# Performance work log

Measured on AMD Instinct MI355X. Metric: run time of the kernel, lower is better.

Reference implementation:

```python
import jax, jax.numpy as jnp
import numpy as np
import math

V, D, L, FF, H, DH, W, DM, T, B = 32000, 1024, 4, 4096, 16, 64, 256, 64, 1024, 1


def rms_norm(x, w):
    return x * jax.lax.rsqrt(jnp.mean(x * x, axis=-1, keepdims=True) + 1e-6) * w


def setup_inputs() -> dict:
    key = jax.random.key(0)
    ks = jax.random.split(key, 16)
    s = 0.02
    return {
        "x": jax.random.randint(ks[0], (B, T), 0, V),
        "embed": jax.random.normal(ks[1], (V, D), jnp.float32) * s,
        "ln_in_w": jnp.ones((D,), jnp.float32),
        "ln1_w": jnp.ones((L, D), jnp.float32),
        "lnd_w": jnp.ones((L, D), jnp.float32),
        "qkv_w": jax.random.normal(ks[2], (L, 3 * H * DH, D), jnp.float32) * s,
        "swa_out_w": jax.random.normal(ks[3], (L, D, H * DH), jnp.float32) * s,
        "k_w": jax.random.normal(ks[4], (L, H * DM, D), jnp.float32) * s,
        "v_w": jax.random.normal(ks[5], (L, H * DM, D), jnp.float32) * s,
        "q_w": jax.random.normal(ks[6], (L, H * DM, D), jnp.float32) * s,
        "beta_w": jax.random.normal(ks[7], (L, H, D), jnp.float32) * s,
        "mem_out_w": jax.random.normal(ks[8], (L, D, H * DM), jnp.float32) * s,
        "gate_w": jax.random.normal(ks[9], (L, D, D), jnp.float32) * s,
        "comb_w": jax.random.normal(ks[10], (L, D, D), jnp.float32) * s,
        "ln2_w": jnp.ones((L, D), jnp.float32),
        "wg": jax.random.normal(ks[11], (L, FF, D), jnp.float32) * s,
        "wu": jax.random.normal(ks[12], (L, FF, D), jnp.float32) * s,
        "wo": jax.random.normal(ks[13], (L, D, FF), jnp.float32) * s,
        "ln_out_w": jnp.ones((D,), jnp.float32),
    }


def _swa(h1, qkv_w, out_w):
    # h1: [B,T,D]
    qkv = jnp.einsum('btd,ed->bte', h1, qkv_w)  # [B,T,3*H*DH]
    q, k, v = jnp.split(qkv, 3, axis=-1)
    q = q.reshape(h1.shape[0], T, H, DH).transpose(0, 2, 1, 3)
    k = k.reshape(h1.shape[0], T, H, DH).transpose(0, 2, 1, 3)
    v = v.reshape(h1.shape[0], T, H, DH).transpose(0, 2, 1, 3)
    scores = jnp.einsum('bhqd,bhkd->bhqk', q, k) * (DH ** -0.5)
    pos = jnp.arange(T)
    dist = pos[:, None] - pos[None, :]
    allowed = (dist >= 0) & (dist < W)  # causal sliding window
    scores = jnp.where(allowed[None, None], scores, -jnp.inf)
    attn = jax.nn.softmax(scores, axis=-1)
    out = jnp.einsum('bhqk,bhkd->bhqd', attn, v)
    out = out.transpose(0, 2, 1, 3).reshape(h1.shape[0], T, H * DH)
    return jnp.einsum('bte,de->btd', out, out_w)


def _delta(h2, k_w, v_w, q_w, beta_w, mem_out_w):
    Bv = h2.shape[0]
    proj = lambda w: jnp.einsum('btd,ed->bte', h2, w).reshape(Bv, T, H, DM).transpose(0, 2, 1, 3)
    keys, values, queries = proj(k_w), proj(v_w), proj(q_w)
    beta = jax.nn.sigmoid(jnp.einsum('btd,hd->bht', h2, beta_w))  # [B,H,T]
    keys = keys / jnp.maximum(jnp.linalg.norm(keys, axis=-1, keepdims=True), 1e-12)
    queries = queries / jnp.maximum(jnp.linalg.norm(queries, axis=-1, keepdims=True), 1e-12)
    log_retain = jnp.log(1.0 - beta + 1e-8)
    cum_log = jnp.cumsum(log_retain, axis=-1)  # [B,H,T]
    log_decay = cum_log[..., :, None] - cum_log[..., None, :]  # [B,H,T,T]
    causal = jnp.triu(jnp.ones((T, T), dtype=bool))  # matches torch.triu mask in source
    decay = jnp.exp(jnp.minimum(log_decay, 0.0)) * causal
    kq = jnp.einsum('bhid,bhjd->bhij', queries, keys) / math.sqrt(DM)
    weights = kq * decay
    out = jnp.einsum('bhij,bhjd->bhid', weights, values)
    out = out + beta[..., None] * values
    out = out.transpose(0, 2, 1, 3).reshape(Bv, T, H * DM)
    return jnp.einsum('bte,de->btd', out, mem_out_w)


def reference(x, embed, ln_in_w, ln1_w, lnd_w, qkv_w, swa_out_w, k_w, v_w, q_w,
              beta_w, mem_out_w, gate_w, comb_w, ln2_w, wg, wu, wo, ln_out_w):
    h = rms_norm(embed[x], ln_in_w)  # [B,T,D]
    for l in range(L):
        h1 = rms_norm(h, ln1_w[l])
        h2 = rms_norm(h, lnd_w[l])
        local = _swa(h1, qkv_w[l], swa_out_w[l])
        global_ctx = _delta(h2, k_w[l], v_w[l], q_w[l], beta_w[l], mem_out_w[l])
        gate = jax.nn.sigmoid(jnp.einsum('btd,ed->bte', h1, gate_w[l]))
        mixed = jnp.einsum('btd,ed->bte', gate * local + (1.0 - gate) * global_ctx, comb_w[l])
        h = h + mixed
        hn = rms_norm(h, ln2_w[l])
        ffn = jnp.einsum('btf,df->btd', jax.nn.silu(jnp.einsum('btd,fd->btf', hn, wg[l])) * jnp.einsum('btd,fd->btf', hn, wu[l]), wo[l])
        h = h + ffn
    logits = jnp.einsum('btd,vd->btv', rms_norm(h, ln_out_w), embed)  # tied head
    return logits
```

## Files before the change

### kernel.cpp

```cpp
#include <hip/hip_runtime.h>

typedef unsigned short u16;
typedef unsigned int   u32;
typedef __attribute__((ext_vector_type(8))) __bf16 bfv8;
typedef __attribute__((ext_vector_type(4))) float  f32x4;

__device__ __forceinline__ u16 f2bf(float f){
  u32 u = __builtin_bit_cast(u32, f);
  return (u16)((u + 0x7FFFu + ((u >> 16) & 1u)) >> 16);
}
__device__ __forceinline__ float bf2f(u16 b){
  return __builtin_bit_cast(float, ((u32)b) << 16);
}
__device__ __forceinline__ u32 pk2(float a, float b){
  return (u32)f2bf(a) | ((u32)f2bf(b) << 16);
}
__device__ __forceinline__ float wsum(float v){
  #pragma unroll
  for (int m = 32; m > 0; m >>= 1) v += __shfl_xor(v, m, 64);
  return v;
}
__device__ __forceinline__ void gload16(const void* g, void* l){
  __builtin_amdgcn_global_load_lds((const __attribute__((address_space(1))) void*)g,
                                   (__attribute__((address_space(3))) void*)l, 16, 0, 0);
}

struct CBatch { const float* s[12]; long long p4[13]; u16* dst; };
__global__ __launch_bounds__(256) void flm_conv(CBatch cb)
{
  const int seg = blockIdx.y;
  const long long base = cb.p4[seg];
  const long long n4 = cb.p4[seg + 1] - base;
  const float* __restrict__ src = cb.s[seg];
  uint2* __restrict__ dst = (uint2*)cb.dst + base;
  for (long long i = (long long)blockIdx.x * 256 + threadIdx.x; i < n4;
       i += (long long)gridDim.x * 256){
    float4 v = ((const float4*)src)[i];
    uint2 p; p.x = pk2(v.x, v.y); p.y = pk2(v.z, v.w);
    dst[i] = p;
  }
}

struct GDesc {
  const u16* A; const float* Bw; float* Cf; u16* Cb;
  int lda, ldb, ldc, kbeg, kend, blk0, epi, pad;
};
struct GBatch { GDesc d[6]; int ng, total; };

template<bool BW>
__global__ __launch_bounds__(512) void flm_mgemm(GBatch gb)
{
  constexpr int LDK = BW ? 64 : 72;
  __shared__ u16 sA[128][LDK];
  __shared__ u16 sB[128][LDK];
  const int tid = threadIdx.x, lane = tid & 63, w = tid >> 6;

  const int T = gb.total, bid = blockIdx.x;
  const int q8 = T >> 3, r8 = T & 7, xc = bid & 7, of = bid >> 3;
  const int lin = (xc < r8 ? xc * (q8 + 1) : r8 * (q8 + 1) + (xc - r8) * q8) + of;
  int di = 0;
  #pragma unroll
  for (int i = 1; i < 6; i++) if (i < gb.ng && lin >= gb.d[i].blk0) di = i;
  const GDesc g = gb.d[di];
  const int local = lin - g.blk0;
  const int row0 = (local & 7) * 128;
  const int col0 = (local >> 3) * 128;
  const int wr = (w >> 2) * 64, wc = (w & 3) * 32;

  f32x4 acc[4][2];
  #pragma unroll
  for (int m = 0; m < 4; m++)
    #pragma unroll
    for (int n = 0; n < 2; n++)
      acc[m][n] = (f32x4){0.f, 0.f, 0.f, 0.f};

  const int csw = ((lane & 7) ^ (lane >> 3)) * 8;
  const u16* B16 = (const u16*)g.Bw;

  for (int k0 = g.kbeg; k0 < g.kend; k0 += 64){
    if constexpr (BW){
      const u16* a0 = g.A + (size_t)(row0 + w*16 + (lane>>3)) * g.lda + k0 + csw;
      const u16* b0 = B16 + (size_t)(col0 + w*16 + (lane>>3)) * g.ldb + k0 + csw;
      gload16(a0,                     &sA[w*16    ][0]);
      gload16(a0 + (size_t)8*g.lda,   &sA[w*16 + 8][0]);
      gload16(b0,                     &sB[w*16    ][0]);
      gload16(b0 + (size_t)8*g.ldb,   &sB[w*16 + 8][0]);
    } else {
      #pragma unroll
      for (int i = 0; i < 2; i++){
        int idx = tid + i * 512;
        int r = idx >> 3, c = (idx & 7) * 8;
        *(uint4*)&sA[r][c] = *(const uint4*)(g.A + (size_t)(row0 + r) * g.lda + k0 + c);
      }
      #pragma unroll
      for (int i = 0; i < 4; i++){
        int idx = tid + i * 512;
        int r = idx >> 4, c = (idx & 15) * 4;
        float4 v = *(const float4*)(g.Bw + (size_t)(col0 + r) * g.ldb + k0 + c);
        uint2 p; p.x = pk2(v.x, v.y); p.y = pk2(v.z, v.w);
        *(uint2*)&sB[r][c] = p;
      }
    }
    __syncthreads();
    #pragma unroll
    for (int kk = 0; kk < 2; kk++){
      bfv8 af[4], bfr[2];
      #pragma unroll
      for (int m = 0; m < 4; m++){
        int row = wr + m*16 + (lane & 15);
        if constexpr (BW){
          int slot = (kk*4 + (lane >> 4)) ^ (row & 7);
          af[m] = *(const bfv8*)((const char*)sA + row*128 + slot*16);
        } else {
          af[m] = *(const bfv8*)&sA[row][kk*32 + (lane >> 4) * 8];
        }
      }
      #pragma unroll
      for (int n = 0; n < 2; n++){
        int row = wc + n*16 + (lane & 15);
        if constexpr (BW){
          int slot = (kk*4 + (lane >> 4)) ^ (row & 7);
          bfr[n] = *(const bfv8*)((const char*)sB + row*128 + slot*16);
        } else {
          bfr[n] = *(const bfv8*)&sB[row][kk*32 + (lane >> 4) * 8];
        }
      }
      #pragma unroll
      for (int m = 0; m < 4; m++)
        #pragma unroll
        for (int n = 0; n < 2; n++)
          acc[m][n] = __builtin_amdgcn_mfma_f32_16x16x32_bf16(af[m], bfr[n], acc[m][n], 0, 0, 0);
    }
    __syncthreads();
  }

  #pragma unroll
  for (int m = 0; m < 4; m++){
    int rbase = row0 + wr + m*16 + (lane >> 4) * 4;
    #pragma unroll
    for (int n = 0; n < 2; n++){
      int col = col0 + wc + n*16 + (lane & 15);
      #pragma unroll
      for (int j = 0; j < 4; j++){
        float v = acc[m][n][j];
        size_t o = (size_t)(rbase + j) * g.ldc + col;
        switch (g.epi){
          case 0: g.Cf[o] = v; break;
          case 1: g.Cb[o] = f2bf(v); break;
          default: atomicAdd(&g.Cf[o], v); break;
        }
      }
    }
  }
}

__global__ __launch_bounds__(256) void flm_mix(
    const float* __restrict__ gr, const float* __restrict__ lo,
    const float* __restrict__ gl, u16* __restrict__ o)
{
  int i = blockIdx.x * 256 + threadIdx.x;
  float4 gv = ((const float4*)gr)[i];
  float4 lv = ((const float4*)lo)[i];
  float4 bv = ((const float4*)gl)[i];
  float sx = 1.f/(1.f+expf(-gv.x)), sy = 1.f/(1.f+expf(-gv.y));
  float sz = 1.f/(1.f+expf(-gv.z)), sw = 1.f/(1.f+expf(-gv.w));
  uint2 p;
  p.x = pk2(sx*lv.x + (1.f-sx)*bv.x, sy*lv.y + (1.f-sy)*bv.y);
  p.y = pk2(sz*lv.z + (1.f-sz)*bv.z, sw*lv.w + (1.f-sw)*bv.w);
  ((uint2*)o)[i] = p;
}

__global__ __launch_bounds__(256) void flm_silu(
    const u16* __restrict__ gg, const u16* __restrict__ uu, u16* __restrict__ o)
{
  int i = blockIdx.x * 256 + threadIdx.x;
  uint2 gv = ((const uint2*)gg)[i];
  uint2 uv = ((const uint2*)uu)[i];
  float g0 = bf2f((u16)gv.x), g1 = bf2f((u16)(gv.x >> 16));
  float g2 = bf2f((u16)gv.y), g3 = bf2f((u16)(gv.y >> 16));
  float u0 = bf2f((u16)uv.x), u1 = bf2f((u16)(uv.x >> 16));
  float u2 = bf2f((u16)uv.y), u3 = bf2f((u16)(uv.y >> 16));
  float a = g0 / (1.f + expf(-g0)) * u0;
  float b = g1 / (1.f + expf(-g1)) * u1;
  float c = g2 / (1.f + expf(-g2)) * u2;
  float d = g3 / (1.f + expf(-g3)) * u3;
  uint2 p; p.x = pk2(a, b); p.y = pk2(c, d);
  ((uint2*)o)[i] = p;
}

__global__ __launch_bounds__(256) void flm_embed(
    const int* __restrict__ x, const float* __restrict__ embed,
    const float* __restrict__ w, float* __restrict__ h)
{
  int t = blockIdx.x, tid = threadIdx.x;
  int tok = x[t];
  float4 v = ((const float4*)(embed + (size_t)tok * 1024))[tid];
  float ss = v.x*v.x + v.y*v.y + v.z*v.z + v.w*v.w;
  ss = wsum(ss);
  __shared__ float red[4];
  if ((tid & 63) == 0) red[tid >> 6] = ss;
  __syncthreads();
  float inv = rsqrtf((red[0]+red[1]+red[2]+red[3]) * (1.f/1024.f) + 1e-6f);
  float4 wv = ((const float4*)w)[tid];
  float4 o; o.x = v.x*inv*wv.x; o.y = v.y*inv*wv.y; o.z = v.z*inv*wv.z; o.w = v.w*inv*wv.w;
  ((float4*)(h + (size_t)t * 1024))[tid] = o;
}

__global__ __launch_bounds__(256) void flm_rms(
    const float* __restrict__ h, const float* __restrict__ w1, const float* __restrict__ w2,
    u16* __restrict__ o1, u16* __restrict__ o2)
{
  int t = blockIdx.x, tid = threadIdx.x;
  float4 v = ((const float4*)(h + (size_t)t * 1024))[tid];
  float ss = v.x*v.x + v.y*v.y + v.z*v.z + v.w*v.w;
  ss = wsum(ss);
  __shared__ float red[4];
  if ((tid & 63) == 0) red[tid >> 6] = ss;
  __syncthreads();
  float inv = rsqrtf((red[0]+red[1]+red[2]+red[3]) * (1.f/1024.f) + 1e-6f);
  {
    float4 wv = ((const float4*)w1)[tid];
    uint2 p; p.x = pk2(v.x*inv*wv.x, v.y*inv*wv.y); p.y = pk2(v.z*inv*wv.z, v.w*inv*wv.w);
    ((uint2*)(o1 + (size_t)t * 1024))[tid] = p;
  }
  if (o2 != nullptr){
    float4 wv = ((const float4*)w2)[tid];
    uint2 p; p.x = pk2(v.x*inv*wv.x, v.y*inv*wv.y); p.y = pk2(v.z*inv*wv.z, v.w*inv*wv.w);
    ((uint2*)(o2 + (size_t)t * 1024))[tid] = p;
  }
}

__global__ __launch_bounds__(64) void flm_betanorm(
    const u16* __restrict__ h2, const float* __restrict__ bw, float* __restrict__ beta,
    u16* __restrict__ keys, u16* __restrict__ queries)
{
  int t = blockIdx.x, lane = threadIdx.x;
  float hv[16];
  #pragma unroll
  for (int i = 0; i < 16; i++) hv[i] = bf2f(h2[(size_t)t*1024 + i*64 + lane]);
  for (int h = 0; h < 16; h++){
    float p = 0.f;
    #pragma unroll
    for (int i = 0; i < 16; i++) p += hv[i] * bw[h*1024 + i*64 + lane];
    p = wsum(p);
    if (lane == 0) beta[t*16 + h] = 1.f / (1.f + expf(-p));
  }
  #pragma unroll
  for (int h = 0; h < 16; h++){
    size_t idx = (size_t)t * 1024 + h * 64 + lane;
    float v = bf2f(keys[idx]);
    float nrm = fmaxf(sqrtf(wsum(v * v)), 1e-12f);
    keys[idx] = f2bf(v / nrm);
    float q = bf2f(queries[idx]);
    float qn = fmaxf(sqrtf(wsum(q * q)), 1e-12f);
    queries[idx] = f2bf(q / qn);
  }
}

__global__ __launch_bounds__(256) void flm_attn(
    const u16* __restrict__ qkv,
    const u16* __restrict__ keys, const u16* __restrict__ values, const u16* __restrict__ queries,
    const float* __restrict__ beta, u16* __restrict__ aout, u16* __restrict__ dout)
{
  __shared__ u16 sK[64][72];
  __shared__ u16 sVt[64][72];
  __shared__ u16 sP[4][16][72];
  const int tid = threadIdx.x, lane = tid & 63, w = tid >> 6;
  const int qt = blockIdx.x, h = blockIdx.y;
  const int base = h * 64;
  const int ri = w*16 + (lane>>4)*4;

  if (blockIdx.z == 0){
    bfv8 aq[2];
    {
      int qrow = qt*64 + w*16 + (lane & 15);
      #pragma unroll
      for (int kk = 0; kk < 2; kk++)
        aq[kk] = *(const bfv8*)(qkv + (size_t)qrow*3072 + base + kk*32 + (lane>>4)*8);
    }
    f32x4 acc_o[4];
    float m_r[4], l_r[4];
    #pragma unroll
    for (int n = 0; n < 4; n++) acc_o[n] = (f32x4){0.f,0.f,0.f,0.f};
    #pragma unroll
    for (int r = 0; r < 4; r++){ m_r[r] = -1e30f; l_r[r] = 0.f; }
    const int jt0 = (qt >= 4) ? qt - 4 : 0;

    for (int jt = qt; jt >= jt0; jt--){
      #pragma unroll
      for (int i = 0; i < 2; i++){
        int idx = tid + i*256;
        int r = idx >> 3, c = (idx & 7) * 8;
        uint4 kv = *(const uint4*)(qkv + (size_t)(jt*64+r)*3072 + 1024 + base + c);
        *(uint4*)&sK[r][c] = kv;
        uint4 vv = *(const uint4*)(qkv + (size_t)(jt*64+r)*3072 + 2048 + base + c);
        u16 tmp[8]; *(uint4*)tmp = vv;
        #pragma unroll
        for (int e = 0; e < 8; e++) sVt[c+e][r] = tmp[e];
      }
      __syncthreads();

      f32x4 sv[4];
      #pragma unroll
      for (int n = 0; n < 4; n++) sv[n] = (f32x4){0.f,0.f,0.f,0.f};
      #pragma unroll
      for (int kk = 0; kk < 2; kk++){
        #pragma unroll
        for (int n = 0; n < 4; n++){
          bfv8 bk = *(const bfv8*)&sK[n*16 + (lane & 15)][(lane>>4)*8 + kk*32];
          sv[n] = __builtin_amdgcn_mfma_f32_16x16x32_bf16(aq[kk], bk, sv[n], 0, 0, 0);
        }
      }
      #pragma unroll
      for (int n = 0; n < 4; n++){
        int cj = n*16 + (lane & 15);
        #pragma unroll
        for (int r = 0; r < 4; r++){
          float s = sv[n][r] * 0.125f;
          if (jt == qt)      { if (cj > ri + r) s = -1e30f; }
          else if (jt == jt0 && qt - jt0 == 4) { if (cj <= ri + r) s = -1e30f; }
          sv[n][r] = s;
        }
      }
      float pv[4][4], scl[4];
      #pragma unroll
      for (int r = 0; r < 4; r++){
        float mx = -1e30f;
        #pragma unroll
        for (int n = 0; n < 4; n++) mx = fmaxf(mx, sv[n][r]);
        #pragma unroll
        for (int m = 1; m < 16; m <<= 1) mx = fmaxf(mx, __shfl_xor(mx, m, 64));
        float mn = fmaxf(m_r[r], mx);
        float sc = expf(m_r[r] - mn);
        m_r[r] = mn; scl[r] = sc;
        float rs = 0.f;
        #pragma unroll
        for (int n = 0; n < 4; n++){ float p = expf(sv[n][r] - mn); pv[n][r] = p; rs += p; }
        #pragma unroll
        for (int m = 1; m < 16; m <<= 1) rs += __shfl_xor(rs, m, 64);
        l_r[r] = l_r[r] * sc + rs;
      }
      #pragma unroll
      for (int n = 0; n < 4; n++){
        #pragma unroll
        for (int r = 0; r < 4; r++){
          acc_o[n][r] *= scl[r];
          sP[w][(lane>>4)*4 + r][n*16 + (lane & 15)] = f2bf(pv[n][r]);
        }
      }
      #pragma unroll
      for (int kk = 0; kk < 2; kk++){
        bfv8 ap = *(const bfv8*)&sP[w][lane & 15][(lane>>4)*8 + kk*32];
        #pragma unroll
        for (int n = 0; n < 4; n++){
          bfv8 bv = *(const bfv8*)&sVt[n*16 + (lane & 15)][(lane>>4)*8 + kk*32];
          acc_o[n] = __builtin_amdgcn_mfma_f32_16x16x32_bf16(ap, bv, acc_o[n], 0, 0, 0);
        }
      }
      __syncthreads();
    }

    #pragma unroll
    for (int n = 0; n < 4; n++){
      int col = base + n*16 + (lane & 15);
      #pragma unroll
      for (int r = 0; r < 4; r++){
        int row = qt*64 + ri + r;
        aout[(size_t)row*1024 + col] = f2bf(acc_o[n][r] / l_r[r]);
      }
    }
  } else {
    bfv8 aq[2];
    {
      int qrow = qt*64 + w*16 + (lane & 15);
      #pragma unroll
      for (int kk = 0; kk < 2; kk++)
        aq[kk] = *(const bfv8*)(queries + (size_t)qrow*1024 + base + kk*32 + (lane>>4)*8);
    }
    f32x4 acc_o[4];
    #pragma unroll
    for (int n = 0; n < 4; n++) acc_o[n] = (f32x4){0.f,0.f,0.f,0.f};

    for (int jt = qt; jt < 16; jt++){
      #pragma unroll
      for (int i = 0; i < 2; i++){
        int idx = tid + i*256;
        int r = idx >> 3, c = (idx & 7) * 8;
        uint4 kv = *(const uint4*)(keys + (size_t)(jt*64+r)*1024 + base + c);
        *(uint4*)&sK[r][c] = kv;
        uint4 vv = *(const uint4*)(values + (size_t)(jt*64+r)*1024 + base + c);
        u16 tmp[8]; *(uint4*)tmp = vv;
        #pragma unroll
        for (int e = 0; e < 8; e++) sVt[c+e][r] = tmp[e];
      }
      __syncthreads();

      f32x4 sv[4];
      #pragma unroll
      for (int n = 0; n < 4; n++) sv[n] = (f32x4){0.f,0.f,0.f,0.f};
      #pragma unroll
      for (int kk = 0; kk < 2; kk++){
        #pragma unroll
        for (int n = 0; n < 4; n++){
          bfv8 bk = *(const bfv8*)&sK[n*16 + (lane & 15)][(lane>>4)*8 + kk*32];
          sv[n] = __builtin_amdgcn_mfma_f32_16x16x32_bf16(aq[kk], bk, sv[n], 0, 0, 0);
        }
      }
      #pragma unroll
      for (int n = 0; n < 4; n++){
        int cj = n*16 + (lane & 15);
        #pragma unroll
        for (int r = 0; r < 4; r++){
          float p = sv[n][r] * 0.125f;
          if (jt == qt && cj < ri + r) p = 0.f;
          sP[w][(lane>>4)*4 + r][n*16 + (lane & 15)] = f2bf(p);
        }
      }
      #pragma unroll
      for (int kk = 0; kk < 2; kk++){
        bfv8 ap = *(const bfv8*)&sP[w][lane & 15][(lane>>4)*8 + kk*32];
        #pragma unroll
        for (int n = 0; n < 4; n++){
          bfv8 bv = *(const bfv8*)&sVt[n*16 + (lane & 15)][(lane>>4)*8 + kk*32];
          acc_o[n] = __builtin_amdgcn_mfma_f32_16x16x32_bf16(ap, bv, acc_o[n], 0, 0, 0);
        }
      }
      __syncthreads();
    }

    #pragma unroll
    for (int n = 0; n < 4; n++){
      int col = base + n*16 + (lane & 15);
      #pragma unroll
      for (int r = 0; r < 4; r++){
        int row = qt*64 + ri + r;
        float b = beta[row*16 + h];
        float v = bf2f(values[(size_t)row*1024 + col]);
        dout[(size_t)row*1024 + col] = f2bf(acc_o[n][r] + b * v);
      }
    }
  }
}

static GDesc mkd(const u16* A, int lda, const float* Bw, int ldb,
                 float* Cf, u16* Cb, int ldc,
                 int kbeg, int kend, int blk0, int epi){
  GDesc d; d.A=A; d.Bw=Bw; d.Cf=Cf; d.Cb=Cb;
  d.lda=lda; d.ldb=ldb; d.ldc=ldc; d.kbeg=kbeg; d.kend=kend; d.blk0=blk0; d.epi=epi; d.pad=0;
  return d;
}

extern "C" void kernel_launch(void* const* d_in, const int* in_sizes, int n_in,
                              void* d_out, int out_size, void* d_ws, size_t ws_size,
                              hipStream_t stream)
{
  (void)in_sizes; (void)n_in; (void)out_size;
  const int*   x        = (const int*)d_in[0];
  const float* embed    = (const float*)d_in[1];
  const float* ln_in_w  = (const float*)d_in[2];
  const float* ln1_w    = (const float*)d_in[3];
  const float* lnd_w    = (const float*)d_in[4];
  const float* qkv_w    = (const float*)d_in[5];
  const float* swa_out_w= (const float*)d_in[6];
  const float* k_w      = (const float*)d_in[7];
  const float* v_w      = (const float*)d_in[8];
  const float* q_w      = (const float*)d_in[9];
  const float* beta_w   = (const float*)d_in[10];
  const float* mem_out_w= (const float*)d_in[11];
  const float* gate_w   = (const float*)d_in[12];
  const float* comb_w   = (const float*)d_in[13];
  const float* ln2_w    = (const float*)d_in[14];
  const float* wg       = (const float*)d_in[15];
  const float* wu       = (const float*)d_in[16];
  const float* wo       = (const float*)d_in[17];
  const float* ln_out_w = (const float*)d_in[18];
  float* out = (float*)d_out;

  char* ws = (char*)d_ws;
  const size_t KB = 1024, MB = 1u << 20;
  float* h       = (float*)(ws + 0);
  u16*   h1      = (u16*)  (ws + 4*MB);
  u16*   h2      = (u16*)  (ws + 6*MB);
  u16*   qkvb    = (u16*)  (ws + 8*MB);
  u16*   keys    = (u16*)  (ws + 14*MB);
  u16*   values  = (u16*)  (ws + 16*MB);
  u16*   queries = (u16*)  (ws + 18*MB);
  float* beta    = (float*)(ws + 20*MB);
  u16*   attn    = (u16*)  (ws + 20*MB + 256*KB);
  u16*   delt    = (u16*)  (ws + 22*MB + 256*KB);
  float* localb  = (float*)(ws + 24*MB + 256*KB);
  float* globb   = (float*)(ws + 28*MB + 256*KB);
  u16*   mcomb   = (u16*)  (ws + 32*MB + 256*KB);
  u16*   hn      = (u16*)  (ws + 36*MB);
  float* gbuf    = (float*)(ws + 40*MB);
  u16*   g16     = (u16*)  (ws + 4*MB);
  u16*   u16b    = (u16*)  (ws + 12*MB);
  u16*   sbuf    = (u16*)  (ws + 36*MB);

  u16* wb = (u16*)(ws + 44*MB);
  size_t off = 0; auto nx = [&](size_t n){ size_t o = off; off += n; return o; };
  const size_t nEmb = 32768000ULL, nQkv = 12582912ULL, nSq = 4194304ULL, nFf = 16777216ULL;
  u16* wemb  = wb + nx(nEmb);
  u16* wqkv  = wb + nx(nQkv);
  u16* wswa  = wb + nx(nSq);
  u16* wk    = wb + nx(nSq);
  u16* wv    = wb + nx(nSq);
  u16* wq    = wb + nx(nSq);
  u16* wmem  = wb + nx(nSq);
  u16* wgate = wb + nx(nSq);
  u16* wcomb = wb + nx(nSq);
  u16* wwg   = wb + nx(nFf);
  u16* wwu   = wb + nx(nFf);
  u16* wwo   = wb + nx(nFf);
  const size_t NEED = 44*MB + off * 2;
  const bool bw = (ws_size >= NEED);

  auto MG = [&](int nblk, GBatch& gbv){
    if (bw) flm_mgemm<true><<<nblk, 512, 0, stream>>>(gbv);
    else    flm_mgemm<false><<<nblk, 512, 0, stream>>>(gbv);
  };

  if (bw){
    CBatch cb;
    const float* srcs[12] = {embed, qkv_w, swa_out_w, k_w, v_w, q_w,
                             mem_out_w, gate_w, comb_w, wg, wu, wo};
    const size_t ns[12] = {nEmb, nQkv, nSq, nSq, nSq, nSq, nSq, nSq, nSq, nFf, nFf, nFf};
    long long acc4 = 0;
    for (int i = 0; i < 12; i++){ cb.s[i] = srcs[i]; cb.p4[i] = acc4; acc4 += (long long)(ns[i] >> 2); }
    cb.p4[12] = acc4; cb.dst = wb;
    flm_conv<<<dim3(1024, 12), 256, 0, stream>>>(cb);
  }

  flm_embed<<<1024, 256, 0, stream>>>(x, embed, ln_in_w, h);

  for (int l = 0; l < 4; l++){
    const size_t lq = (size_t)l * 3145728, ls = (size_t)l * 1048576, lf = (size_t)l * 4194304;
    const float* Wqkv  = bw ? (const float*)(wqkv  + lq) : qkv_w     + lq;
    const float* Wk    = bw ? (const float*)(wk    + ls) : k_w       + ls;
    const float* Wv    = bw ? (const float*)(wv    + ls) : v_w       + ls;
    const float* Wq    = bw ? (const float*)(wq    + ls) : q_w       + ls;
    const float* Wswa  = bw ? (const float*)(wswa  + ls) : swa_out_w + ls;
    const float* Wmem  = bw ? (const float*)(wmem  + ls) : mem_out_w + ls;
    const float* Wgate = bw ? (const float*)(wgate + ls) : gate_w    + ls;
    const float* Wcomb = bw ? (const float*)(wcomb + ls) : comb_w    + ls;
    const float* Wwg   = bw ? (const float*)(wwg   + lf) : wg        + lf;
    const float* Wwu   = bw ? (const float*)(wwu   + lf) : wu        + lf;
    const float* Wwo   = bw ? (const float*)(wwo   + lf) : wo        + lf;

    flm_rms<<<1024, 256, 0, stream>>>(h, ln1_w + l*1024, lnd_w + l*1024, h1, h2);

    {
      GBatch gb;
      gb.d[0] = mkd(h1, 1024, Wqkv, 1024, nullptr, qkvb, 3072, 0, 1024, 0, 1);
      gb.d[1] = mkd(h2, 1024, Wk, 1024, nullptr, keys, 1024, 0, 1024, 192, 1);
      gb.d[2] = mkd(h2, 1024, Wv, 1024, nullptr, values, 1024, 0, 1024, 256, 1);
      gb.d[3] = mkd(h2, 1024, Wq, 1024, nullptr, queries, 1024, 0, 1024, 320, 1);
      gb.d[4] = mkd(h1, 1024, Wgate, 1024, gbuf, nullptr, 1024, 0, 1024, 384, 0);
      gb.d[5] = gb.d[4]; gb.d[5].blk0 = 0x7fffffff;
      gb.ng = 5; gb.total = 448;
      MG(448, gb);
    }
    flm_betanorm<<<1024, 64, 0, stream>>>(h2, beta_w + (size_t)l*16*1024, beta, keys, queries);
    flm_attn<<<dim3(16, 16, 2), 256, 0, stream>>>(qkvb, keys, values, queries, beta, attn, delt);

    {
      GBatch gb;
      gb.d[0] = mkd(attn, 1024, Wswa, 1024, localb, nullptr, 1024, 0, 1024, 0, 0);
      gb.d[1] = mkd(delt, 1024, Wmem, 1024, globb, nullptr, 1024, 0, 1024, 64, 0);
      gb.d[2] = gb.d[1]; gb.d[2].blk0 = 0x7fffffff;
      gb.d[3] = gb.d[2]; gb.d[4] = gb.d[2]; gb.d[5] = gb.d[2];
      gb.ng = 2; gb.total = 128;
      MG(128, gb);
    }
    flm_mix<<<1024, 256, 0, stream>>>(gbuf, localb, globb, mcomb);
    {
      GBatch gb;
      gb.d[0] = mkd(mcomb, 1024, Wcomb, 1024, h, nullptr, 1024, 0, 512, 0, 5);
      gb.d[1] = mkd(mcomb, 1024, Wcomb, 1024, h, nullptr, 1024, 512, 1024, 64, 5);
      gb.d[2] = gb.d[1]; gb.d[2].blk0 = 0x7fffffff;
      gb.d[3] = gb.d[2]; gb.d[4] = gb.d[2]; gb.d[5] = gb.d[2];
      gb.ng = 2; gb.total = 128;
      MG(128, gb);
    }
    flm_rms<<<1024, 256, 0, stream>>>(h, ln2_w + l*1024, nullptr, hn, nullptr);
    {
      GBatch gb;
      gb.d[0] = mkd(hn, 1024, Wwg, 1024, nullptr, g16, 4096, 0, 1024, 0, 1);
      gb.d[1] = mkd(hn, 1024, Wwu, 1024, nullptr, u16b, 4096, 0, 1024, 256, 1);
      gb.d[2] = gb.d[1]; gb.d[2].blk0 = 0x7fffffff;
      gb.d[3] = gb.d[2]; gb.d[4] = gb.d[2]; gb.d[5] = gb.d[2];
      gb.ng = 2; gb.total = 512;
      MG(512, gb);
    }
    flm_silu<<<4096, 256, 0, stream>>>(g16, u16b, sbuf);
    {
      GBatch gb;
      for (int s = 0; s < 4; s++)
        gb.d[s] = mkd(sbuf, 4096, Wwo, 4096, h, nullptr, 1024, s*1024, (s+1)*1024, s*64, 5);
      gb.d[4] = gb.d[3]; gb.d[4].blk0 = 0x7fffffff;
      gb.d[5] = gb.d[4];
      gb.ng = 4; gb.total = 256;
      MG(256, gb);
    }
  }

  flm_rms<<<1024, 256, 0, stream>>>(h, ln_out_w, nullptr, hn, nullptr);
  {
    GBatch gb;
    gb.d[0] = mkd(hn, 1024, bw ? (const float*)wemb : embed, 1024, out, nullptr, 32000,
                  0, 1024, 0, 0);
    gb.d[1] = gb.d[0]; gb.d[1].blk0 = 0x7fffffff;
    gb.d[2] = gb.d[1]; gb.d[3] = gb.d[1]; gb.d[4] = gb.d[1]; gb.d[5] = gb.d[1];
    gb.ng = 1; gb.total = 2000;
    MG(2000, gb);
  }
}
```

Before: 1.007 ms.

## Fuse gate-mix and SiLU into GEMM A-loads, split-K out-proj, balance delta attention

The elementwise gate/mix kernel and the SiLU*up kernel are folded into the A-operand staging of the following GEMMs (AF=1 and AF=2), which removes two launches and their intermediate round trips. The SWA/memory output projections become split-K with partial sums kept in separate buffers that the fused mix adds together. The delta-attention blocks now each process query tiles p and 15-p, so the triangular work per block is balanced, and the weight conversion kernel uses wider nontemporal loads and stores. The trade-off is that A-tile loads become synchronous register loads with expf computed inside the GEMM loop, and each K-step reads five fp32 arrays.

```diff
diff --git a/kernel.cpp b/kernel.cpp
--- a/kernel.cpp
+++ b/kernel.cpp
@@ -4,6 +4,7 @@
 typedef unsigned int   u32;
 typedef __attribute__((ext_vector_type(8))) __bf16 bfv8;
 typedef __attribute__((ext_vector_type(4))) float  f32x4;
+typedef __attribute__((ext_vector_type(4))) u32    u32x4;
 
 __device__ __forceinline__ u16 f2bf(float f){
   u32 u = __builtin_bit_cast(u32, f);
@@ -30,24 +31,28 @@
 {
   const int seg = blockIdx.y;
   const long long base = cb.p4[seg];
-  const long long n4 = cb.p4[seg + 1] - base;
-  const float* __restrict__ src = cb.s[seg];
-  uint2* __restrict__ dst = (uint2*)cb.dst + base;
-  for (long long i = (long long)blockIdx.x * 256 + threadIdx.x; i < n4;
+  const long long n8 = (cb.p4[seg + 1] - base) >> 1;
+  const f32x4* __restrict__ src = (const f32x4*)cb.s[seg];
+  u32x4* __restrict__ dst = (u32x4*)cb.dst + (base >> 1);
+  for (long long i = (long long)blockIdx.x * 256 + threadIdx.x; i < n8;
        i += (long long)gridDim.x * 256){
-    float4 v = ((const float4*)src)[i];
-    uint2 p; p.x = pk2(v.x, v.y); p.y = pk2(v.z, v.w);
-    dst[i] = p;
+    f32x4 v0 = __builtin_nontemporal_load(src + 2*i);
+    f32x4 v1 = __builtin_nontemporal_load(src + 2*i + 1);
+    u32x4 p;
+    p.x = pk2(v0.x, v0.y); p.y = pk2(v0.z, v0.w);
+    p.z = pk2(v1.x, v1.y); p.w = pk2(v1.z, v1.w);
+    __builtin_nontemporal_store(p, dst + i);
   }
 }
 
 struct GDesc {
   const u16* A; const float* Bw; float* Cf; u16* Cb;
+  const void* xa; const void* xb; const void* xc; const void* xd; const void* xe;
   int lda, ldb, ldc, kbeg, kend, blk0, epi, pad;
 };
 struct GBatch { GDesc d[6]; int ng, total; };
 
-template<bool BW>
+template<bool BW, int AF>
 __global__ __launch_bounds__(512) void flm_mgemm(GBatch gb)
 {
   constexpr int LDK = BW ? 64 : 72;
@@ -75,16 +80,54 @@
       acc[m][n] = (f32x4){0.f, 0.f, 0.f, 0.f};
 
   const int csw = ((lane & 7) ^ (lane >> 3)) * 8;
+  const int arow = w*16 + (lane >> 3);
   const u16* B16 = (const u16*)g.Bw;
 
   for (int k0 = g.kbeg; k0 < g.kend; k0 += 64){
     if constexpr (BW){
-      const u16* a0 = g.A + (size_t)(row0 + w*16 + (lane>>3)) * g.lda + k0 + csw;
-      const u16* b0 = B16 + (size_t)(col0 + w*16 + (lane>>3)) * g.ldb + k0 + csw;
-      gload16(a0,                     &sA[w*16    ][0]);
-      gload16(a0 + (size_t)8*g.lda,   &sA[w*16 + 8][0]);
-      gload16(b0,                     &sB[w*16    ][0]);
-      gload16(b0 + (size_t)8*g.ldb,   &sB[w*16 + 8][0]);
+      if constexpr (AF == 0){
+        const u16* a0 = g.A + (size_t)(row0 + arow) * g.lda + k0 + csw;
+        gload16(a0,                   &sA[w*16    ][0]);
+        gload16(a0 + (size_t)8*g.lda, &sA[w*16 + 8][0]);
+      } else if constexpr (AF == 1){
+        #pragma unroll
+        for (int half = 0; half < 2; half++){
+          int rr = arow + half*8;
+          size_t base = (size_t)(row0 + rr) * 1024 + k0 + csw;
+          const float* G  = (const float*)g.xa + base;
+          const float* L0 = (const float*)g.xb + base;
+          const float* L1 = (const float*)g.xc + base;
+          const float* H0 = (const float*)g.xd + base;
+          const float* H1 = (const float*)g.xe + base;
+          u16 t8[8];
+          #pragma unroll
+          for (int e = 0; e < 8; e++){
+            float s = 1.f / (1.f + expf(-G[e]));
+            t8[e] = f2bf(s * (L0[e] + L1[e]) + (1.f - s) * (H0[e] + H1[e]));
+          }
+          *(uint4*)&sA[rr][(lane & 7) * 8] = *(uint4*)t8;
+        }
+      } else {
+        #pragma unroll
+        for (int half = 0; half < 2; half++){
+          int rr = arow + half*8;
+          size_t base = (size_t)(row0 + rr) * g.lda + k0 + csw;
+          uint4 gv = *(const uint4*)((const u16*)g.xa + base);
+          uint4 uv = *(const uint4*)((const u16*)g.xb + base);
+          const u16* gp = (const u16*)&gv;
+          const u16* up = (const u16*)&uv;
+          u16 t8[8];
+          #pragma unroll
+          for (int e = 0; e < 8; e++){
+            float gg = bf2f(gp[e]), uu = bf2f(up[e]);
+            t8[e] = f2bf(gg / (1.f + expf(-gg)) * uu);
+          }
+          *(uint4*)&sA[rr][(lane & 7) * 8] = *(uint4*)t8;
+        }
+      }
+      const u16* b0 = B16 + (size_t)(col0 + arow) * g.ldb + k0 + csw;
+      gload16(b0,                   &sB[w*16    ][0]);
+      gload16(b0 + (size_t)8*g.ldb, &sB[w*16 + 8][0]);
     } else {
       #pragma unroll
       for (int i = 0; i < 2; i++){
@@ -266,11 +309,12 @@
   __shared__ u16 sVt[64][72];
   __shared__ u16 sP[4][16][72];
   const int tid = threadIdx.x, lane = tid & 63, w = tid >> 6;
-  const int qt = blockIdx.x, h = blockIdx.y;
+  const int bx = blockIdx.x, h = blockIdx.y;
   const int base = h * 64;
   const int ri = w*16 + (lane>>4)*4;
 
-  if (blockIdx.z == 0){
+  if (bx < 16){
+    const int qt = bx;
     bfv8 aq[2];
     {
       int qrow = qt*64 + w*16 + (lane & 15);
@@ -370,73 +414,78 @@
       }
     }
   } else {
-    bfv8 aq[2];
-    {
-      int qrow = qt*64 + w*16 + (lane & 15);
-      #pragma unroll
-      for (int kk = 0; kk < 2; kk++)
-        aq[kk] = *(const bfv8*)(queries + (size_t)qrow*1024 + base + kk*32 + (lane>>4)*8);
-    }
-    f32x4 acc_o[4];
-    #pragma unroll
-    for (int n = 0; n < 4; n++) acc_o[n] = (f32x4){0.f,0.f,0.f,0.f};
-
-    for (int jt = qt; jt < 16; jt++){
-      #pragma unroll
-      for (int i = 0; i < 2; i++){
-        int idx = tid + i*256;
-        int r = idx >> 3, c = (idx & 7) * 8;
-        uint4 kv = *(const uint4*)(keys + (size_t)(jt*64+r)*1024 + base + c);
-        *(uint4*)&sK[r][c] = kv;
-        uint4 vv = *(const uint4*)(values + (size_t)(jt*64+r)*1024 + base + c);
-        u16 tmp[8]; *(uint4*)tmp = vv;
-        #pragma unroll
-        for (int e = 0; e < 8; e++) sVt[c+e][r] = tmp[e];
-      }
-      __syncthreads();
-
-      f32x4 sv[4];
-      #pragma unroll
-      for (int n = 0; n < 4; n++) sv[n] = (f32x4){0.f,0.f,0.f,0.f};
-      #pragma unroll
-      for (int kk = 0; kk < 2; kk++){
+    const int p = bx - 16;
+    #pragma unroll 1
+    for (int sel = 0; sel < 2; sel++){
+      const int qt = sel ? (15 - p) : p;
+      bfv8 aq[2];
+      {
+        int qrow = qt*64 + w*16 + (lane & 15);
+        #pragma unroll
+        for (int kk = 0; kk < 2; kk++)
+          aq[kk] = *(const bfv8*)(queries + (size_t)qrow*1024 + base + kk*32 + (lane>>4)*8);
+      }
+      f32x4 acc_o[4];
+      #pragma unroll
+      for (int n = 0; n < 4; n++) acc_o[n] = (f32x4){0.f,0.f,0.f,0.f};
+
+      for (int jt = qt; jt < 16; jt++){
+        #pragma unroll
+        for (int i = 0; i < 2; i++){
+          int idx = tid + i*256;
+          int r = idx >> 3, c = (idx & 7) * 8;
+          uint4 kv = *(const uint4*)(keys + (size_t)(jt*64+r)*1024 + base + c);
+          *(uint4*)&sK[r][c] = kv;
+          uint4 vv = *(const uint4*)(values + (size_t)(jt*64+r)*1024 + base + c);
+          u16 tmp[8]; *(uint4*)tmp = vv;
+          #pragma unroll
+          for (int e = 0; e < 8; e++) sVt[c+e][r] = tmp[e];
+        }
+        __syncthreads();
+
+        f32x4 sv[4];
+        #pragma unroll
+        for (int n = 0; n < 4; n++) sv[n] = (f32x4){0.f,0.f,0.f,0.f};
+        #pragma unroll
+        for (int kk = 0; kk < 2; kk++){
+          #pragma unroll
+          for (int n = 0; n < 4; n++){
+            bfv8 bk = *(const bfv8*)&sK[n*16 + (lane & 15)][(lane>>4)*8 + kk*32];
+            sv[n] = __builtin_amdgcn_mfma_f32_16x16x32_bf16(aq[kk], bk, sv[n], 0, 0, 0);
+          }
+        }
         #pragma unroll
         for (int n = 0; n < 4; n++){
-          bfv8 bk = *(const bfv8*)&sK[n*16 + (lane & 15)][(lane>>4)*8 + kk*32];
-          sv[n] = __builtin_amdgcn_mfma_f32_16x16x32_bf16(aq[kk], bk, sv[n], 0, 0, 0);
-        }
-      }
+          int cj = n*16 + (lane & 15);
+          #pragma unroll
+          for (int r = 0; r < 4; r++){
+            float pp = sv[n][r] * 0.125f;
+            if (jt == qt && cj < ri + r) pp = 0.f;
+            sP[w][(lane>>4)*4 + r][n*16 + (lane & 15)] = f2bf(pp);
+          }
+        }
+        #pragma unroll
+        for (int kk = 0; kk < 2; kk++){
+          bfv8 ap = *(const bfv8*)&sP[w][lane & 15][(lane>>4)*8 + kk*32];
+          #pragma unroll
+          for (int n = 0; n < 4; n++){
+            bfv8 bv = *(const bfv8*)&sVt[n*16 + (lane & 15)][(lane>>4)*8 + kk*32];
+            acc_o[n] = __builtin_amdgcn_mfma_f32_16x16x32_bf16(ap, bv, acc_o[n], 0, 0, 0);
+          }
+        }
+        __syncthreads();
+      }
+
       #pragma unroll
       for (int n = 0; n < 4; n++){
-        int cj = n*16 + (lane & 15);
+        int col = base + n*16 + (lane & 15);
         #pragma unroll
         for (int r = 0; r < 4; r++){
-          float p = sv[n][r] * 0.125f;
-          if (jt == qt && cj < ri + r) p = 0.f;
-          sP[w][(lane>>4)*4 + r][n*16 + (lane & 15)] = f2bf(p);
-        }
-      }
-      #pragma unroll
-      for (int kk = 0; kk < 2; kk++){
-        bfv8 ap = *(const bfv8*)&sP[w][lane & 15][(lane>>4)*8 + kk*32];
-        #pragma unroll
-        for (int n = 0; n < 4; n++){
-          bfv8 bv = *(const bfv8*)&sVt[n*16 + (lane & 15)][(lane>>4)*8 + kk*32];
-          acc_o[n] = __builtin_amdgcn_mfma_f32_16x16x32_bf16(ap, bv, acc_o[n], 0, 0, 0);
-        }
-      }
-      __syncthreads();
-    }
-
-    #pragma unroll
-    for (int n = 0; n < 4; n++){
-      int col = base + n*16 + (lane & 15);
-      #pragma unroll
-      for (int r = 0; r < 4; r++){
-        int row = qt*64 + ri + r;
-        float b = beta[row*16 + h];
-        float v = bf2f(values[(size_t)row*1024 + col]);
-        dout[(size_t)row*1024 + col] = f2bf(acc_o[n][r] + b * v);
+          int row = qt*64 + ri + r;
+          float b = beta[row*16 + h];
+          float v = bf2f(values[(size_t)row*1024 + col]);
+          dout[(size_t)row*1024 + col] = f2bf(acc_o[n][r] + b * v);
+        }
       }
     }
   }
@@ -444,8 +493,12 @@
 
 static GDesc mkd(const u16* A, int lda, const float* Bw, int ldb,
                  float* Cf, u16* Cb, int ldc,
-                 int kbeg, int kend, int blk0, int epi){
+                 int kbeg, int kend, int blk0, int epi,
+                 const void* xa = nullptr, const void* xb = nullptr,
+                 const void* xc = nullptr, const void* xd = nullptr,
+                 const void* xe = nullptr){
   GDesc d; d.A=A; d.Bw=Bw; d.Cf=Cf; d.Cb=Cb;
+  d.xa=xa; d.xb=xb; d.xc=xc; d.xd=xd; d.xe=xe;
   d.lda=lda; d.ldb=ldb; d.ldc=ldc; d.kbeg=kbeg; d.kend=kend; d.blk0=blk0; d.epi=epi; d.pad=0;
   return d;
 }
@@ -488,16 +541,18 @@
   float* beta    = (float*)(ws + 20*MB);
   u16*   attn    = (u16*)  (ws + 20*MB + 256*KB);
   u16*   delt    = (u16*)  (ws + 22*MB + 256*KB);
-  float* localb  = (float*)(ws + 24*MB + 256*KB);
-  float* globb   = (float*)(ws + 28*MB + 256*KB);
-  u16*   mcomb   = (u16*)  (ws + 32*MB + 256*KB);
-  u16*   hn      = (u16*)  (ws + 36*MB);
-  float* gbuf    = (float*)(ws + 40*MB);
+  float* lo0     = (float*)(ws + 24*MB + 256*KB);
+  float* lo1     = (float*)(ws + 28*MB + 256*KB);
+  float* gl0     = (float*)(ws + 32*MB + 256*KB);
+  float* gl1     = (float*)(ws + 36*MB + 256*KB);
+  float* gbuf    = (float*)(ws + 40*MB + 256*KB);
+  u16*   mcomb   = (u16*)  (ws + 44*MB + 256*KB);
+  u16*   hn      = (u16*)  (ws + 46*MB + 256*KB);
   u16*   g16     = (u16*)  (ws + 4*MB);
   u16*   u16b    = (u16*)  (ws + 12*MB);
-  u16*   sbuf    = (u16*)  (ws + 36*MB);
-
-  u16* wb = (u16*)(ws + 44*MB);
+  u16*   sbuf    = (u16*)  (ws + 20*MB);
+
+  u16* wb = (u16*)(ws + 48*MB + 512*KB);
   size_t off = 0; auto nx = [&](size_t n){ size_t o = off; off += n; return o; };
   const size_t nEmb = 32768000ULL, nQkv = 12582912ULL, nSq = 4194304ULL, nFf = 16777216ULL;
   u16* wemb  = wb + nx(nEmb);
@@ -512,12 +567,12 @@
   u16* wwg   = wb + nx(nFf);
   u16* wwu   = wb + nx(nFf);
   u16* wwo   = wb + nx(nFf);
-  const size_t NEED = 44*MB + off * 2;
+  const size_t NEED = 48*MB + 512*KB + off * 2;
   const bool bw = (ws_size >= NEED);
 
-  auto MG = [&](int nblk, GBatch& gbv){
-    if (bw) flm_mgemm<true><<<nblk, 512, 0, stream>>>(gbv);
-    else    flm_mgemm<false><<<nblk, 512, 0, stream>>>(gbv);
+  auto MG0 = [&](int nblk, GBatch& gbv){
+    if (bw) flm_mgemm<true, 0><<<nblk, 512, 0, stream>>>(gbv);
+    else    flm_mgemm<false, 0><<<nblk, 512, 0, stream>>>(gbv);
   };
 
   if (bw){
@@ -558,30 +613,52 @@
       gb.d[4] = mkd(h1, 1024, Wgate, 1024, gbuf, nullptr, 1024, 0, 1024, 384, 0);
       gb.d[5] = gb.d[4]; gb.d[5].blk0 = 0x7fffffff;
       gb.ng = 5; gb.total = 448;
-      MG(448, gb);
+      MG0(448, gb);
     }
     flm_betanorm<<<1024, 64, 0, stream>>>(h2, beta_w + (size_t)l*16*1024, beta, keys, queries);
-    flm_attn<<<dim3(16, 16, 2), 256, 0, stream>>>(qkvb, keys, values, queries, beta, attn, delt);
-
-    {
+    flm_attn<<<dim3(24, 16), 256, 0, stream>>>(qkvb, keys, values, queries, beta, attn, delt);
+
+    if (bw){
+      {
+        GBatch gb;
+        gb.d[0] = mkd(attn, 1024, Wswa, 1024, lo0, nullptr, 1024, 0,   512,  0,   0);
+        gb.d[1] = mkd(attn, 1024, Wswa, 1024, lo1, nullptr, 1024, 512, 1024, 64,  0);
+        gb.d[2] = mkd(delt, 1024, Wmem, 1024, gl0, nullptr, 1024, 0,   512,  128, 0);
+        gb.d[3] = mkd(delt, 1024, Wmem, 1024, gl1, nullptr, 1024, 512, 1024, 192, 0);
+        gb.d[4] = gb.d[3]; gb.d[4].blk0 = 0x7fffffff;
+        gb.d[5] = gb.d[4];
+        gb.ng = 4; gb.total = 256;
+        flm_mgemm<true, 0><<<256, 512, 0, stream>>>(gb);
+      }
+      {
+        GBatch gb;
+        gb.d[0] = mkd(nullptr, 1024, Wcomb, 1024, h, nullptr, 1024, 0,   512,  0,  5,
+                      gbuf, lo0, lo1, gl0, gl1);
+        gb.d[1] = mkd(nullptr, 1024, Wcomb, 1024, h, nullptr, 1024, 512, 1024, 64, 5,
+                      gbuf, lo0, lo1, gl0, gl1);
+        gb.d[2] = gb.d[1]; gb.d[2].blk0 = 0x7fffffff;
+        gb.d[3] = gb.d[2]; gb.d[4] = gb.d[2]; gb.d[5] = gb.d[2];
+        gb.ng = 2; gb.total = 128;
+        flm_mgemm<true, 1><<<128, 512, 0, stream>>>(gb);
+      }
+    } else {
       GBatch gb;
-      gb.d[0] = mkd(attn, 1024, Wswa, 1024, localb, nullptr, 1024, 0, 1024, 0, 0);
-      gb.d[1] = mkd(delt, 1024, Wmem, 1024, globb, nullptr, 1024, 0, 1024, 64, 0);
+      gb.d[0] = mkd(attn, 1024, Wswa, 1024, lo0, nullptr, 1024, 0, 1024, 0, 0);
+      gb.d[1] = mkd(delt, 1024, Wmem, 1024, gl0, nullptr, 1024, 0, 1024, 64, 0);
       gb.d[2] = gb.d[1]; gb.d[2].blk0 = 0x7fffffff;
       gb.d[3] = gb.d[2]; gb.d[4] = gb.d[2]; gb.d[5] = gb.d[2];
       gb.ng = 2; gb.total = 128;
-      MG(128, gb);
-    }
-    flm_mix<<<1024, 256, 0, stream>>>(gbuf, localb, globb, mcomb);
-    {
-      GBatch gb;
-      gb.d[0] = mkd(mcomb, 1024, Wcomb, 1024, h, nullptr, 1024, 0, 512, 0, 5);
-      gb.d[1] = mkd(mcomb, 1024, Wcomb, 1024, h, nullptr, 1024, 512, 1024, 64, 5);
-      gb.d[2] = gb.d[1]; gb.d[2].blk0 = 0x7fffffff;
-      gb.d[3] = gb.d[2]; gb.d[4] = gb.d[2]; gb.d[5] = gb.d[2];
-      gb.ng = 2; gb.total = 128;
-      MG(128, gb);
-    }
+      MG0(128, gb);
+      flm_mix<<<1024, 256, 0, stream>>>(gbuf, lo0, gl0, mcomb);
+      GBatch gc;
+      gc.d[0] = mkd(mcomb, 1024, Wcomb, 1024, h, nullptr, 1024, 0, 512, 0, 5);
+      gc.d[1] = mkd(mcomb, 1024, Wcomb, 1024, h, nullptr, 1024, 512, 1024, 64, 5);
+      gc.d[2] = gc.d[1]; gc.d[2].blk0 = 0x7fffffff;
+      gc.d[3] = gc.d[2]; gc.d[4] = gc.d[2]; gc.d[5] = gc.d[2];
+      gc.ng = 2; gc.total = 128;
+      MG0(128, gc);
+    }
+
     flm_rms<<<1024, 256, 0, stream>>>(h, ln2_w + l*1024, nullptr, hn, nullptr);
     {
       GBatch gb;
@@ -590,17 +667,26 @@
       gb.d[2] = gb.d[1]; gb.d[2].blk0 = 0x7fffffff;
       gb.d[3] = gb.d[2]; gb.d[4] = gb.d[2]; gb.d[5] = gb.d[2];
       gb.ng = 2; gb.total = 512;
-      MG(512, gb);
-    }
-    flm_silu<<<4096, 256, 0, stream>>>(g16, u16b, sbuf);
-    {
+      MG0(512, gb);
+    }
+    if (bw){
+      GBatch gb;
+      for (int s = 0; s < 4; s++)
+        gb.d[s] = mkd(nullptr, 4096, Wwo, 4096, h, nullptr, 1024, s*1024, (s+1)*1024, s*64, 5,
+                      g16, u16b);
+      gb.d[4] = gb.d[3]; gb.d[4].blk0 = 0x7fffffff;
+      gb.d[5] = gb.d[4];
+      gb.ng = 4; gb.total = 256;
+      flm_mgemm<true, 2><<<256, 512, 0, stream>>>(gb);
+    } else {
+      flm_silu<<<4096, 256, 0, stream>>>(g16, u16b, sbuf);
       GBatch gb;
       for (int s = 0; s < 4; s++)
         gb.d[s] = mkd(sbuf, 4096, Wwo, 4096, h, nullptr, 1024, s*1024, (s+1)*1024, s*64, 5);
       gb.d[4] = gb.d[3]; gb.d[4].blk0 = 0x7fffffff;
       gb.d[5] = gb.d[4];
       gb.ng = 4; gb.total = 256;
-      MG(256, gb);
+      MG0(256, gb);
     }
   }
 
@@ -612,6 +698,6 @@
     gb.d[1] = gb.d[0]; gb.d[1].blk0 = 0x7fffffff;
     gb.d[2] = gb.d[1]; gb.d[3] = gb.d[1]; gb.d[4] = gb.d[1]; gb.d[5] = gb.d[1];
     gb.ng = 1; gb.total = 2000;
-    MG(2000, gb);
-  }
-}
+    MG0(2000, gb);
+  }
+}
```

After: 1.222 ms. 1.21x slower.
